# Performance work log

Measured on AMD Instinct MI355X. Metric: run time of the kernel, lower is better.

## Reference

```python
import jax, jax.numpy as jnp
import numpy as np

M = 16384            # total tokens in batch (s)
MAX_RANK = 64        # K, max LoRA rank
NUM_SLICES = 2       # fused output slices (<=3 per kernel static_assert)
OUTPUT_DIM = 4096    # N
NUM_LORA = 8         # number of adapters
NUM_SEGMENTS = 8     # contiguous logical segments, one adapter each


def setup_inputs() -> dict:
    key = jax.random.key(0)
    k1, k2, k3, k4, k5 = jax.random.split(key, 5)
    x = jax.random.normal(k1, (M, NUM_SLICES * MAX_RANK), dtype=jnp.float32)
    weights = jax.random.normal(k2, (NUM_LORA, OUTPUT_DIM, MAX_RANK), dtype=jnp.float32) * 0.02
    # equal-length segments covering all M tokens
    seg_indptr = jnp.arange(NUM_SEGMENTS + 1, dtype=jnp.int32) * (M // NUM_SEGMENTS)
    weight_indices = jax.random.randint(k3, (NUM_SEGMENTS,), 0, NUM_LORA, dtype=jnp.int32)
    # variable per-adapter ranks, including a rank-0 (no-op) adapter
    lora_ranks = jnp.array([64, 32, 16, 0, 64, 48, 64, 32], dtype=jnp.int32)
    scalings = jax.random.uniform(k4, (NUM_LORA,), dtype=jnp.float32, minval=0.25, maxval=2.0)
    permutation = jax.random.permutation(k5, M).astype(jnp.int32)
    slice_offsets = jnp.array([0, OUTPUT_DIM // 2, OUTPUT_DIM], dtype=jnp.int32)
    return dict(x=x, weights=weights, seg_indptr=seg_indptr,
                weight_indices=weight_indices, lora_ranks=lora_ranks,
                scalings=scalings, permutation=permutation,
                slice_offsets=slice_offsets, num_segments=NUM_SEGMENTS)


def reference(x, weights, seg_indptr, weight_indices, lora_ranks, scalings,
              permutation, slice_offsets, num_segments):
    M_, D = x.shape
    num_lora, out_dim, max_rank = weights.shape
    num_slices = slice_offsets.shape[0] - 1
    xp = x[permutation]                     # rows in logical (segment) order: (M, D)
    logical = jnp.arange(M_)
    kk = jnp.arange(max_rank)
    nn = jnp.arange(out_dim)
    acc = jnp.zeros((M_, out_dim), dtype=x.dtype)   # accumulated in logical order
    for s in range(num_segments):
        w = weight_indices[s]
        r = lora_ranks[w]                   # actual rank of this segment's adapter
        scal = scalings[w].astype(x.dtype)
        in_seg = (logical >= seg_indptr[s]) & (logical < seg_indptr[s + 1]) & (r > 0)
        W = weights[w]                      # (OUTPUT_DIM, MAX_RANK)
        seg_acc = jnp.zeros((M_, out_dim), dtype=x.dtype)
        for j in range(num_slices):
            kmask = kk < r                  # only first r of MAX_RANK columns are live
            cols = jnp.where(kmask, j * r + kk, 0)   # x packed at slice_id * cur_rank
            xsub = xp[:, cols] * kmask.astype(x.dtype)        # (M, MAX_RANK)
            nmask = ((nn >= slice_offsets[j]) & (nn < slice_offsets[j + 1])).astype(x.dtype)
            seg_acc = seg_acc + (xsub @ W.T) * (scal * nmask)  # (M, OUTPUT_DIM)
        acc = acc + jnp.where(in_seg[:, None], seg_acc, 0.0)
    # scatter back from logical order to physical row positions
    out = jnp.zeros((M_, out_dim), dtype=x.dtype).at[permutation].add(acc)
    return out
```

## Files before the change

### kernel.cpp

```cpp
#include <hip/hip_runtime.h>

typedef float  f32x2v __attribute__((ext_vector_type(2)));
typedef float  f32x4  __attribute__((ext_vector_type(4)));
typedef __bf16 bf16x8 __attribute__((ext_vector_type(8)));

constexpr int D_IN   = 128;
constexpr int KMAX   = 64;
constexpr int N_OUT  = 4096;
constexpr int NSLICE = 2;

constexpr int BM = 128;
constexpr int BN = 128;
constexpr int THREADS = 256;

constexpr size_t WBF_OFF = 0;
constexpr size_t XBF_OFF = 8u << 20;

__device__ __forceinline__ unsigned short f2bf(float f) {
    unsigned u = __builtin_bit_cast(unsigned, f);
    u += 0x7fffu + ((u >> 16) & 1u);
    return (unsigned short)(u >> 16);
}
__device__ __forceinline__ unsigned pk2(float a, float b) {
    return (unsigned)f2bf(a) | ((unsigned)f2bf(b) << 16);
}

__global__ __launch_bounds__(256)
void conv_w(const float* __restrict__ w, unsigned* __restrict__ wbf, int npairs) {
    int i = blockIdx.x * 256 + threadIdx.x;
    if (i >= npairs) return;
    f32x2v v = *(const f32x2v*)&w[(size_t)i * 2];
    wbf[i] = pk2(v.x, v.y);
}

__global__ __launch_bounds__(256)
void conv_x(const float* __restrict__ x,
            const int*   __restrict__ seg_indptr,
            const int*   __restrict__ weight_indices,
            const int*   __restrict__ lora_ranks,
            const float* __restrict__ scalings,
            const int*   __restrict__ permutation,
            unsigned* __restrict__ xbf,
            int num_segments, int m_tok)
{
    const int idx = blockIdx.x * 256 + threadIdx.x;
    const int l   = idx >> 6;
    if (l >= m_tok) return;
    const int c   = (idx & 63) * 2;
    const int j   = c >> 6;
    const int k   = c & 63;

    int s = 0;
    for (int i = 0; i < num_segments; ++i)
        if (l >= seg_indptr[i] && l < seg_indptr[i + 1]) s = i;
    const int   w    = weight_indices[s];
    const int   r    = lora_ranks[w];
    const float scal = scalings[w];

    const int p = permutation[l];
    float v0 = 0.f, v1 = 0.f;
    if (k < r)     v0 = scal * x[(size_t)p * D_IN + j * r + k];
    if (k + 1 < r) v1 = scal * x[(size_t)p * D_IN + j * r + k + 1];
    xbf[idx] = pk2(v0, v1);
}

__global__ __launch_bounds__(THREADS, 4)
void lora_mfma(const __bf16* __restrict__ xbf,
               const __bf16* __restrict__ wbf,
               const int*    __restrict__ seg_indptr,
               const int*    __restrict__ weight_indices,
               const int*    __restrict__ permutation,
               const int*    __restrict__ slice_offsets,
               float* __restrict__ out,
               int num_segments, int n_slices)
{
    __shared__ int Ps[BM];

    const int t    = threadIdx.x;
    const int row0 = blockIdx.y * BM;
    const int col0 = blockIdx.x * BN;

    if (t < BM) Ps[t] = permutation[row0 + t];
    __syncthreads();

    int s = 0;
    for (int i = 0; i < num_segments; ++i)
        if (row0 >= seg_indptr[i] && row0 < seg_indptr[i + 1]) s = i;
    const int w = weight_indices[s];

    int j = 0;
    for (int i = 1; i < n_slices; ++i) j += (col0 >= slice_offsets[i]);

    const int lane = t & 63;
    const int wv   = t >> 6;
    const int wm   = wv & 1;
    const int wn   = wv >> 1;
    const int quad = lane >> 4;
    const int l16  = lane & 15;

    const __bf16* __restrict__ Xb = xbf + ((size_t)(row0 + wm * 64 + l16) * NSLICE + j) * KMAX;
    const __bf16* __restrict__ Wb = wbf + ((size_t)w * N_OUT + col0 + wn * 64 + l16) * KMAX;

    f32x4 acc[4][4];
    #pragma unroll
    for (int a = 0; a < 4; ++a)
        #pragma unroll
        for (int b = 0; b < 4; ++b) acc[a][b] = {0.f, 0.f, 0.f, 0.f};

    #pragma unroll
    for (int kk = 0; kk < 2; ++kk) {
        const int kof = kk * 32 + quad * 8;
        bf16x8 af[4], bfr[4];
        #pragma unroll
        for (int mt = 0; mt < 4; ++mt)
            af[mt] = *(const bf16x8*)&Xb[(size_t)(mt * 16) * NSLICE * KMAX + kof];
        #pragma unroll
        for (int nt = 0; nt < 4; ++nt)
            bfr[nt] = *(const bf16x8*)&Wb[(size_t)(nt * 16) * KMAX + kof];
        #pragma unroll
        for (int mt = 0; mt < 4; ++mt)
            #pragma unroll
            for (int nt = 0; nt < 4; ++nt)
                acc[mt][nt] = __builtin_amdgcn_mfma_f32_16x16x32_bf16(
                    af[mt], bfr[nt], acc[mt][nt], 0, 0, 0);
    }

    #pragma unroll
    for (int mt = 0; mt < 4; ++mt) {
        #pragma unroll
        for (int i = 0; i < 4; ++i) {
            const int m = wm * 64 + mt * 16 + quad * 4 + i;
            float* op = &out[(size_t)Ps[m] * N_OUT + col0 + wn * 64 + l16];
            #pragma unroll
            for (int nt = 0; nt < 4; ++nt)
                op[nt * 16] = acc[mt][nt][i];
        }
    }
}

extern "C" void kernel_launch(void* const* d_in, const int* in_sizes, int n_in,
                              void* d_out, int out_size, void* d_ws, size_t ws_size,
                              hipStream_t stream) {
    (void)n_in; (void)out_size; (void)ws_size;
    const float* x              = (const float*)d_in[0];
    const float* weights        = (const float*)d_in[1];
    const int*   seg_indptr     = (const int*)d_in[2];
    const int*   weight_indices = (const int*)d_in[3];
    const int*   lora_ranks     = (const int*)d_in[4];
    const float* scalings       = (const float*)d_in[5];
    const int*   permutation    = (const int*)d_in[6];
    const int*   slice_offsets  = (const int*)d_in[7];
    float*       out            = (float*)d_out;

    const int num_segments = in_sizes[2] - 1;
    const int n_slices     = in_sizes[7] - 1;
    const int m_tok        = in_sizes[6];
    const int w_elems      = in_sizes[1];

    unsigned* wbf = (unsigned*)((char*)d_ws + WBF_OFF);
    unsigned* xbf = (unsigned*)((char*)d_ws + XBF_OFF);

    const int wpairs = w_elems / 2;
    conv_w<<<(wpairs + 255) / 256, 256, 0, stream>>>(weights, wbf, wpairs);

    const int xthreads = m_tok * (NSLICE * KMAX / 2);
    conv_x<<<(xthreads + 255) / 256, 256, 0, stream>>>(
        x, seg_indptr, weight_indices, lora_ranks, scalings, permutation,
        xbf, num_segments, m_tok);

    dim3 grid(N_OUT / BN, m_tok / BM);
    lora_mfma<<<grid, THREADS, 0, stream>>>(
        (const __bf16*)xbf, (const __bf16*)wbf, seg_indptr, weight_indices,
        permutation, slice_offsets, out, num_segments, n_slices);
}
```

Baseline: 308.3 us.

## Fuse weight and activation conversion kernels and retile MFMA GEMM to 64x512

Merges the two bf16 conversion kernels into one launch that handles 8 elements per thread with 16-byte vector loads and stores. The GEMM tile changes from 128x128 with 256 threads to 64x512 with 512 threads. Each wave now covers 16 rows by 256 columns, loading its A fragment once and streaming 16 B tiles. This is meant to cut launch overhead and conversion instruction count and improve weight reuse, at the cost of the A operand being reused less and the per-wave output scatter pattern changing.

```diff
diff --git a/kernel.cpp b/kernel.cpp
--- a/kernel.cpp
+++ b/kernel.cpp
@@ -1,6 +1,5 @@
 #include <hip/hip_runtime.h>
 
-typedef float  f32x2v __attribute__((ext_vector_type(2)));
 typedef float  f32x4  __attribute__((ext_vector_type(4)));
 typedef __bf16 bf16x8 __attribute__((ext_vector_type(8)));
 
@@ -9,9 +8,9 @@
 constexpr int N_OUT  = 4096;
 constexpr int NSLICE = 2;
 
-constexpr int BM = 128;
-constexpr int BN = 128;
-constexpr int THREADS = 256;
+constexpr int BM = 64;
+constexpr int BN = 512;
+constexpr int THREADS = 512;
 
 constexpr size_t WBF_OFF = 0;
 constexpr size_t XBF_OFF = 8u << 20;
@@ -26,42 +25,59 @@
 }
 
 __global__ __launch_bounds__(256)
-void conv_w(const float* __restrict__ w, unsigned* __restrict__ wbf, int npairs) {
-    int i = blockIdx.x * 256 + threadIdx.x;
-    if (i >= npairs) return;
-    f32x2v v = *(const f32x2v*)&w[(size_t)i * 2];
-    wbf[i] = pk2(v.x, v.y);
-}
+void conv_all(const float* __restrict__ w, uint4* __restrict__ wbf4, int wvec,
+              const float* __restrict__ x,
+              const int*   __restrict__ seg_indptr,
+              const int*   __restrict__ weight_indices,
+              const int*   __restrict__ lora_ranks,
+              const float* __restrict__ scalings,
+              const int*   __restrict__ permutation,
+              uint4* __restrict__ xbf4,
+              int num_segments, int m_tok, int wblocks)
+{
+    const int bid = blockIdx.x;
+    if (bid < wblocks) {
+        const int i = bid * 256 + threadIdx.x;
+        if (i >= wvec) return;
+        const float* src = w + (size_t)i * 8;
+        f32x4 a = *(const f32x4*)src;
+        f32x4 b = *(const f32x4*)(src + 4);
+        uint4 o;
+        o.x = pk2(a.x, a.y); o.y = pk2(a.z, a.w);
+        o.z = pk2(b.x, b.y); o.w = pk2(b.z, b.w);
+        wbf4[i] = o;
+    } else {
+        const int idx = (bid - wblocks) * 256 + threadIdx.x;
+        if (idx >= m_tok * 16) return;
+        const int l = idx >> 4;
+        const int c = (idx & 15) * 8;
+        const int j = c >> 6;
+        const int k = c & 63;
 
-__global__ __launch_bounds__(256)
-void conv_x(const float* __restrict__ x,
-            const int*   __restrict__ seg_indptr,
-            const int*   __restrict__ weight_indices,
-            const int*   __restrict__ lora_ranks,
-            const float* __restrict__ scalings,
-            const int*   __restrict__ permutation,
-            unsigned* __restrict__ xbf,
-            int num_segments, int m_tok)
-{
-    const int idx = blockIdx.x * 256 + threadIdx.x;
-    const int l   = idx >> 6;
-    if (l >= m_tok) return;
-    const int c   = (idx & 63) * 2;
-    const int j   = c >> 6;
-    const int k   = c & 63;
+        int s = 0;
+        for (int i = 0; i < num_segments; ++i)
+            if (l >= seg_indptr[i] && l < seg_indptr[i + 1]) s = i;
+        const int   wi   = weight_indices[s];
+        const int   r    = lora_ranks[wi];
+        const float scal = scalings[wi];
 
-    int s = 0;
-    for (int i = 0; i < num_segments; ++i)
-        if (l >= seg_indptr[i] && l < seg_indptr[i + 1]) s = i;
-    const int   w    = weight_indices[s];
-    const int   r    = lora_ranks[w];
-    const float scal = scalings[w];
-
-    const int p = permutation[l];
-    float v0 = 0.f, v1 = 0.f;
-    if (k < r)     v0 = scal * x[(size_t)p * D_IN + j * r + k];
-    if (k + 1 < r) v1 = scal * x[(size_t)p * D_IN + j * r + k + 1];
-    xbf[idx] = pk2(v0, v1);
+        const float* base = x + (size_t)permutation[l] * D_IN + j * r;
+        uint4 o;
+        if (k + 8 <= r && ((j * r) & 3) == 0) {
+            f32x4 a = *(const f32x4*)(base + k);
+            f32x4 b = *(const f32x4*)(base + k + 4);
+            o.x = pk2(scal * a.x, scal * a.y); o.y = pk2(scal * a.z, scal * a.w);
+            o.z = pk2(scal * b.x, scal * b.y); o.w = pk2(scal * b.z, scal * b.w);
+        } else {
+            float v[8];
+            #pragma unroll
+            for (int e = 0; e < 8; ++e)
+                v[e] = (k + e < r) ? scal * base[k + e] : 0.f;
+            o.x = pk2(v[0], v[1]); o.y = pk2(v[2], v[3]);
+            o.z = pk2(v[4], v[5]); o.w = pk2(v[6], v[7]);
+        }
+        xbf4[idx] = o;
+    }
 }
 
 __global__ __launch_bounds__(THREADS, 4)
@@ -93,48 +109,39 @@
 
     const int lane = t & 63;
     const int wv   = t >> 6;
-    const int wm   = wv & 1;
-    const int wn   = wv >> 1;
+    const int wn   = wv & 1;
+    const int wm   = wv >> 1;
     const int quad = lane >> 4;
     const int l16  = lane & 15;
 
-    const __bf16* __restrict__ Xb = xbf + ((size_t)(row0 + wm * 64 + l16) * NSLICE + j) * KMAX;
-    const __bf16* __restrict__ Wb = wbf + ((size_t)w * N_OUT + col0 + wn * 64 + l16) * KMAX;
+    const __bf16* __restrict__ Xb =
+        xbf + ((size_t)(row0 + wm * 16 + l16) * NSLICE + j) * KMAX;
+    const __bf16* __restrict__ Wb =
+        wbf + ((size_t)w * N_OUT + col0 + wn * 256 + l16) * KMAX + quad * 8;
 
-    f32x4 acc[4][4];
+    f32x4 acc[16];
     #pragma unroll
-    for (int a = 0; a < 4; ++a)
-        #pragma unroll
-        for (int b = 0; b < 4; ++b) acc[a][b] = {0.f, 0.f, 0.f, 0.f};
+    for (int nt = 0; nt < 16; ++nt) acc[nt] = {0.f, 0.f, 0.f, 0.f};
+
+    const bf16x8 af0 = *(const bf16x8*)&Xb[quad * 8];
+    const bf16x8 af1 = *(const bf16x8*)&Xb[32 + quad * 8];
 
     #pragma unroll
-    for (int kk = 0; kk < 2; ++kk) {
-        const int kof = kk * 32 + quad * 8;
-        bf16x8 af[4], bfr[4];
-        #pragma unroll
-        for (int mt = 0; mt < 4; ++mt)
-            af[mt] = *(const bf16x8*)&Xb[(size_t)(mt * 16) * NSLICE * KMAX + kof];
-        #pragma unroll
-        for (int nt = 0; nt < 4; ++nt)
-            bfr[nt] = *(const bf16x8*)&Wb[(size_t)(nt * 16) * KMAX + kof];
-        #pragma unroll
-        for (int mt = 0; mt < 4; ++mt)
-            #pragma unroll
-            for (int nt = 0; nt < 4; ++nt)
-                acc[mt][nt] = __builtin_amdgcn_mfma_f32_16x16x32_bf16(
-                    af[mt], bfr[nt], acc[mt][nt], 0, 0, 0);
+    for (int nt = 0; nt < 16; ++nt) {
+        const __bf16* wp = Wb + (size_t)nt * 16 * KMAX;
+        bf16x8 b0 = *(const bf16x8*)&wp[0];
+        bf16x8 b1 = *(const bf16x8*)&wp[32];
+        acc[nt] = __builtin_amdgcn_mfma_f32_16x16x32_bf16(af0, b0, acc[nt], 0, 0, 0);
+        acc[nt] = __builtin_amdgcn_mfma_f32_16x16x32_bf16(af1, b1, acc[nt], 0, 0, 0);
     }
 
     #pragma unroll
-    for (int mt = 0; mt < 4; ++mt) {
+    for (int i = 0; i < 4; ++i) {
+        const int m = wm * 16 + quad * 4 + i;
+        float* op = &out[(size_t)Ps[m] * N_OUT + col0 + wn * 256 + l16];
         #pragma unroll
-        for (int i = 0; i < 4; ++i) {
-            const int m = wm * 64 + mt * 16 + quad * 4 + i;
-            float* op = &out[(size_t)Ps[m] * N_OUT + col0 + wn * 64 + l16];
-            #pragma unroll
-            for (int nt = 0; nt < 4; ++nt)
-                op[nt * 16] = acc[mt][nt][i];
-        }
+        for (int nt = 0; nt < 16; ++nt)
+            op[nt * 16] = acc[nt][i];
     }
 }
 
@@ -157,16 +164,17 @@
     const int m_tok        = in_sizes[6];
     const int w_elems      = in_sizes[1];
 
-    unsigned* wbf = (unsigned*)((char*)d_ws + WBF_OFF);
-    unsigned* xbf = (unsigned*)((char*)d_ws + XBF_OFF);
+    uint4* wbf = (uint4*)((char*)d_ws + WBF_OFF);
+    uint4* xbf = (uint4*)((char*)d_ws + XBF_OFF);
 
-    const int wpairs = w_elems / 2;
-    conv_w<<<(wpairs + 255) / 256, 256, 0, stream>>>(weights, wbf, wpairs);
+    const int wvec    = w_elems / 8;
+    const int wblocks = (wvec + 255) / 256;
+    const int xthr    = m_tok * 16;
+    const int xblocks = (xthr + 255) / 256;
 
-    const int xthreads = m_tok * (NSLICE * KMAX / 2);
-    conv_x<<<(xthreads + 255) / 256, 256, 0, stream>>>(
-        x, seg_indptr, weight_indices, lora_ranks, scalings, permutation,
-        xbf, num_segments, m_tok);
+    conv_all<<<wblocks + xblocks, 256, 0, stream>>>(
+        weights, wbf, wvec, x, seg_indptr, weight_indices, lora_ranks,
+        scalings, permutation, xbf, num_segments, m_tok, wblocks);
 
     dim3 grid(N_OUT / BN, m_tok / BM);
     lora_mfma<<<grid, THREADS, 0, stream>>>(
```

Result: slower. 326.2 us (+5.8%).
